# Optimization experiments

Measured on AMD Instinct MI355X. Metric: run time of the kernel, lower is better.

## Reference

```python
import jax, jax.numpy as jnp
import numpy as np

N_OCTAVES = 32
N_SAMPLES = 32768
SAMPLERATE = 22050
MIN_HZ = 20
MAX_HZ = 3000
BASE_RESONANCE = 0.01


def setup_inputs() -> dict:
    key = jax.random.key(0)
    k1, k2, k3 = jax.random.split(key, 3)
    B, E = 4, 16
    return {
        "f0": jax.random.uniform(k1, (B, E, 1), dtype=jnp.float32),
        "decay_coefficients": jax.random.normal(k2, (B, E, 1), dtype=jnp.float32),
        "freq_spacing": jax.random.uniform(k3, (B, E, 1), dtype=jnp.float32),
    }


def reference(f0, decay_coefficients, freq_spacing):
    B, E, _ = f0.shape
    min_freq = MIN_HZ / (SAMPLERATE // 2)
    max_freq = MAX_HZ / (SAMPLERATE // 2)
    freq_range = max_freq - min_freq

    f0 = jnp.abs(f0)  # (B, E, 1)

    # exponential_decay: note the forward applies sigmoid BEFORE calling
    # exponential_decay, which applies sigmoid again -> double sigmoid.
    dv = jax.nn.sigmoid(jax.nn.sigmoid(decay_coefficients))  # (B, E, 1)
    resonance_factor = (1.0 - BASE_RESONANCE) * 0.99
    d = BASE_RESONANCE + dv * resonance_factor  # (B, E, 1)
    log_d = jnp.broadcast_to(jnp.log(d + 1e-12), (B, E, N_OCTAVES))
    # interpolate(size=n_frames) with in==out size is the identity, so skip it.
    exp_decays = jnp.exp(jnp.cumsum(log_d, axis=-1))  # (B, E, O)

    f0 = (min_freq + f0 * freq_range) * np.pi  # (B, E, 1)
    factors = jnp.cumsum(jnp.broadcast_to(freq_spacing, (B, E, N_OCTAVES)), axis=-1)
    f0s = f0 * factors  # (B, E, O)
    f0s = f0s * (f0s < 1).astype(f0s.dtype)  # mask partials above Nyquist

    # cumsum of a constant per-sample frequency == freq * (sample_index + 1)
    t = jnp.arange(1, N_SAMPLES + 1, dtype=f0s.dtype)  # (S,)
    phase = f0s[..., None] * t  # (B, E, O, S)
    osc = jnp.sin(phase) * exp_decays[..., None]  # (B, E, O, S)

    osc = jnp.sum(osc, axis=2)  # (B, E, S)
    mx = jnp.max(jnp.abs(osc), axis=-1, keepdims=True)
    return osc / (mx + 1e-8)
```

## Files before the change

kernel.cpp:

```cpp
#include <hip/hip_runtime.h>
#include <math.h>

#define N_OCT  32
#define N_SMP  32768
#define N_PAIR 64
#define BPP    32

__global__ __launch_bounds__(256) void f0res_osc(
    const float* __restrict__ f0_in,
    const float* __restrict__ dec_in,
    const float* __restrict__ fs_in,
    float* __restrict__ out,
    float* __restrict__ bmax)
{
    __shared__ __align__(16) float sw[N_OCT];
    __shared__ __align__(16) float sa[N_OCT];
    __shared__ int s_ng;

    const int pair = blockIdx.x >> 5;
    const int blk  = blockIdx.x & (BPP - 1);
    const int tid  = threadIdx.x;

    if (tid < N_OCT) {
        const float minf   = (float)(20.0 / 11025.0);
        const float frange = (float)(3000.0 / 11025.0 - 20.0 / 11025.0);
        const float pif    = 3.14159265358979323846f;
        const float INV2PI = 0.15915494309189535f;

        float f0 = fabsf(f0_in[pair]);
        float fs = fs_in[pair];
        float x  = dec_in[pair];

        float s1 = 1.0f / (1.0f + expf(-x));
        float s2 = 1.0f / (1.0f + expf(-s1));
        float d  = 0.01f + s2 * (float)(0.99 * 0.99);
        float ld = logf(d + 1e-12f);
        float f0p = (minf + f0 * frange) * pif;

        float fac = 0.0f, acl = 0.0f, myfac = 0.0f, myacl = 0.0f;
#pragma unroll
        for (int o = 0; o < N_OCT; ++o) {
            fac += fs;
            acl += ld;
            if (o == tid) { myfac = fac; myacl = acl; }
        }
        float f0s = f0p * myfac;
        const bool act = (f0s < 1.0f);
        sw[tid] = act ? f0s * INV2PI : 0.0f;
        sa[tid] = expf(myacl);

        unsigned long long bal = __ballot(act);
        if (tid == 0) s_ng = (__popcll(bal) + 3) >> 2;
    }
    __syncthreads();

    const int ng = s_ng;

    const int   s0 = (blk << 10) + tid;
    const float t0 = (float)(s0 + 1);
    const float t1 = (float)(s0 + 257);
    const float t2 = (float)(s0 + 513);
    const float t3 = (float)(s0 + 769);

    float acc0 = 0.0f, acc1 = 0.0f, acc2 = 0.0f, acc3 = 0.0f;

    const float4* w4 = (const float4*)sw;
    const float4* a4 = (const float4*)sa;
    for (int i = 0; i < ng; ++i) {
        const float4 wv = w4[i];
        const float4 av = a4[i];
        const float wr[4] = { wv.x, wv.y, wv.z, wv.w };
        const float ar[4] = { av.x, av.y, av.z, av.w };
#pragma unroll
        for (int j = 0; j < 4; ++j) {
            const float w = wr[j], a = ar[j];
            acc0 = fmaf(a, __builtin_amdgcn_sinf(__builtin_amdgcn_fractf(w * t0)), acc0);
            acc1 = fmaf(a, __builtin_amdgcn_sinf(__builtin_amdgcn_fractf(w * t1)), acc1);
            acc2 = fmaf(a, __builtin_amdgcn_sinf(__builtin_amdgcn_fractf(w * t2)), acc2);
            acc3 = fmaf(a, __builtin_amdgcn_sinf(__builtin_amdgcn_fractf(w * t3)), acc3);
        }
    }

    float* op = out + pair * N_SMP + s0;
    op[0]   = acc0;
    op[256] = acc1;
    op[512] = acc2;
    op[768] = acc3;

    float av_ = fmaxf(fmaxf(fabsf(acc0), fabsf(acc1)),
                      fmaxf(fabsf(acc2), fabsf(acc3)));
#pragma unroll
    for (int m = 32; m >= 1; m >>= 1)
        av_ = fmaxf(av_, __shfl_xor(av_, m, 64));
    __shared__ float wm[4];
    if ((tid & 63) == 0) wm[tid >> 6] = av_;
    __syncthreads();
    if (tid == 0)
        bmax[pair * BPP + blk] = fmaxf(fmaxf(wm[0], wm[1]), fmaxf(wm[2], wm[3]));
}

__global__ __launch_bounds__(256) void f0res_norm(
    float* __restrict__ out, const float* __restrict__ bmax)
{
    const int pair = blockIdx.x >> 5;
    const int tid  = threadIdx.x;

    float v = (tid < BPP) ? bmax[pair * BPP + tid] : 0.0f;
#pragma unroll
    for (int m = 16; m >= 1; m >>= 1)
        v = fmaxf(v, __shfl_xor(v, m, 64));
    __shared__ float smx;
    if (tid == 0) smx = v;
    __syncthreads();
    const float inv = 1.0f / (smx + 1e-8f);

    const int idx = ((blockIdx.x & 31) << 8) + tid;
    float4* o4 = (float4*)(out + pair * N_SMP);
    float4 val = o4[idx];
    val.x *= inv; val.y *= inv; val.z *= inv; val.w *= inv;
    o4[idx] = val;
}

extern "C" void kernel_launch(void* const* d_in, const int* in_sizes, int n_in,
                              void* d_out, int out_size, void* d_ws, size_t ws_size,
                              hipStream_t stream) {
    const float* f0  = (const float*)d_in[0];
    const float* dec = (const float*)d_in[1];
    const float* fs  = (const float*)d_in[2];
    float* out = (float*)d_out;

    float* bmax = (float*)d_ws;

    f0res_osc <<<N_PAIR * BPP, 256, 0, stream>>>(f0, dec, fs, out, bmax);
    f0res_norm<<<N_PAIR * 32,  256, 0, stream>>>(out, bmax);
}
```

Before: 69.66 us.

## Fuse oscillator and normalization into one cooperative kernel with grid sync

Merges the oscillator synthesis and normalization kernels into a single cooperative launch. Each block now computes 8 samples per thread and keeps them in registers. After a grid-wide sync it reads the per-pair maxima and writes the normalized output directly. This removes the second kernel launch and a full global read-modify-write of the output. In exchange it adds grid-sync overhead, requires all 1024 blocks to be co-resident, and halves the block count per pair.

```diff
diff --git a/kernel.cpp b/kernel.cpp
--- a/kernel.cpp
+++ b/kernel.cpp
@@ -1,12 +1,14 @@
 #include <hip/hip_runtime.h>
+#include <hip/hip_cooperative_groups.h>
 #include <math.h>
 
 #define N_OCT  32
 #define N_SMP  32768
 #define N_PAIR 64
-#define BPP    32
+#define BPP    16
+#define NBLK   (N_PAIR * BPP)
 
-__global__ __launch_bounds__(256) void f0res_osc(
+__global__ __launch_bounds__(256, 4) void f0res_fused(
     const float* __restrict__ f0_in,
     const float* __restrict__ dec_in,
     const float* __restrict__ fs_in,
@@ -16,8 +18,9 @@
     __shared__ __align__(16) float sw[N_OCT];
     __shared__ __align__(16) float sa[N_OCT];
     __shared__ int s_ng;
+    __shared__ float wm[4];
 
-    const int pair = blockIdx.x >> 5;
+    const int pair = blockIdx.x >> 4;
     const int blk  = blockIdx.x & (BPP - 1);
     const int tid  = threadIdx.x;
 
@@ -56,13 +59,13 @@
 
     const int ng = s_ng;
 
-    const int   s0 = (blk << 10) + tid;
-    const float t0 = (float)(s0 + 1);
-    const float t1 = (float)(s0 + 257);
-    const float t2 = (float)(s0 + 513);
-    const float t3 = (float)(s0 + 769);
-
-    float acc0 = 0.0f, acc1 = 0.0f, acc2 = 0.0f, acc3 = 0.0f;
+    const int s0 = (blk << 11) + tid;
+    float t[8], acc[8];
+#pragma unroll
+    for (int k = 0; k < 8; ++k) {
+        t[k]   = (float)(s0 + 1 + (k << 8));
+        acc[k] = 0.0f;
+    }
 
     const float4* w4 = (const float4*)sw;
     const float4* a4 = (const float4*)sa;
@@ -74,51 +77,39 @@
 #pragma unroll
         for (int j = 0; j < 4; ++j) {
             const float w = wr[j], a = ar[j];
-            acc0 = fmaf(a, __builtin_amdgcn_sinf(__builtin_amdgcn_fractf(w * t0)), acc0);
-            acc1 = fmaf(a, __builtin_amdgcn_sinf(__builtin_amdgcn_fractf(w * t1)), acc1);
-            acc2 = fmaf(a, __builtin_amdgcn_sinf(__builtin_amdgcn_fractf(w * t2)), acc2);
-            acc3 = fmaf(a, __builtin_amdgcn_sinf(__builtin_amdgcn_fractf(w * t3)), acc3);
+#pragma unroll
+            for (int k = 0; k < 8; ++k)
+                acc[k] = fmaf(a, __builtin_amdgcn_sinf(
+                                     __builtin_amdgcn_fractf(w * t[k])), acc[k]);
         }
     }
 
-    float* op = out + pair * N_SMP + s0;
-    op[0]   = acc0;
-    op[256] = acc1;
-    op[512] = acc2;
-    op[768] = acc3;
-
-    float av_ = fmaxf(fmaxf(fabsf(acc0), fabsf(acc1)),
-                      fmaxf(fabsf(acc2), fabsf(acc3)));
+    float av_ = 0.0f;
+#pragma unroll
+    for (int k = 0; k < 8; ++k) av_ = fmaxf(av_, fabsf(acc[k]));
 #pragma unroll
     for (int m = 32; m >= 1; m >>= 1)
         av_ = fmaxf(av_, __shfl_xor(av_, m, 64));
-    __shared__ float wm[4];
     if ((tid & 63) == 0) wm[tid >> 6] = av_;
     __syncthreads();
-    if (tid == 0)
-        bmax[pair * BPP + blk] = fmaxf(fmaxf(wm[0], wm[1]), fmaxf(wm[2], wm[3]));
-}
+    if (tid == 0) {
+        bmax[(pair << 4) + blk] =
+            fmaxf(fmaxf(wm[0], wm[1]), fmaxf(wm[2], wm[3]));
+        __threadfence();
+    }
 
-__global__ __launch_bounds__(256) void f0res_norm(
-    float* __restrict__ out, const float* __restrict__ bmax)
-{
-    const int pair = blockIdx.x >> 5;
-    const int tid  = threadIdx.x;
+    cooperative_groups::this_grid().sync();
 
-    float v = (tid < BPP) ? bmax[pair * BPP + tid] : 0.0f;
+    float v = bmax[(pair << 4) + (tid & 15)];
 #pragma unroll
-    for (int m = 16; m >= 1; m >>= 1)
+    for (int m = 8; m >= 1; m >>= 1)
         v = fmaxf(v, __shfl_xor(v, m, 64));
-    __shared__ float smx;
-    if (tid == 0) smx = v;
-    __syncthreads();
-    const float inv = 1.0f / (smx + 1e-8f);
+    const float inv = 1.0f / (v + 1e-8f);
 
-    const int idx = ((blockIdx.x & 31) << 8) + tid;
-    float4* o4 = (float4*)(out + pair * N_SMP);
-    float4 val = o4[idx];
-    val.x *= inv; val.y *= inv; val.z *= inv; val.w *= inv;
-    o4[idx] = val;
+    float* op = out + pair * N_SMP + s0;
+#pragma unroll
+    for (int k = 0; k < 8; ++k)
+        op[k << 8] = acc[k] * inv;
 }
 
 extern "C" void kernel_launch(void* const* d_in, const int* in_sizes, int n_in,
@@ -127,10 +118,11 @@
     const float* f0  = (const float*)d_in[0];
     const float* dec = (const float*)d_in[1];
     const float* fs  = (const float*)d_in[2];
-    float* out = (float*)d_out;
-
+    float* out  = (float*)d_out;
     float* bmax = (float*)d_ws;
 
-    f0res_osc <<<N_PAIR * BPP, 256, 0, stream>>>(f0, dec, fs, out, bmax);
-    f0res_norm<<<N_PAIR * 32,  256, 0, stream>>>(out, bmax);
+    void* args[] = { (void*)&f0, (void*)&dec, (void*)&fs,
+                     (void*)&out, (void*)&bmax };
+    hipLaunchCooperativeKernel((void*)f0res_fused,
+                               dim3(NBLK), dim3(256), args, 0, stream);
 }
```

New measurement: 145.3 us. 2.09x slower.

## Fuse normalization into oscillator kernel via last-block atomic counter

Applied to the files above, without the earlier changes.

Drops the separate normalization kernel launch. Each block publishes its block max and increments a per-pair atomic counter, and the last block to finish for a pair reduces the maxima and rescales the whole 32K-sample row. The counter is reset by subtracting 32, and a probe value read from the workspace serves as the baseline. The aim is to remove launch overhead and the global barrier between kernels. In exchange, the rescale of each row is serialized onto a single block, and correctness depends on the workspace counter state and memory ordering.

```diff
diff --git a/kernel.cpp b/kernel.cpp
--- a/kernel.cpp
+++ b/kernel.cpp
@@ -11,15 +11,25 @@
     const float* __restrict__ dec_in,
     const float* __restrict__ fs_in,
     float* __restrict__ out,
-    float* __restrict__ bmax)
+    unsigned int* __restrict__ ws)
 {
     __shared__ __align__(16) float sw[N_OCT];
     __shared__ __align__(16) float sa[N_OCT];
     __shared__ int s_ng;
+    __shared__ unsigned int s_P;
+    __shared__ float wm[4];
+    __shared__ int s_last;
+    __shared__ float s_inv;
 
     const int pair = blockIdx.x >> 5;
     const int blk  = blockIdx.x & (BPP - 1);
     const int tid  = threadIdx.x;
+
+    unsigned int* cnt   = ws;
+    float*        bmax  = (float*)(ws + 256);
+    const unsigned int* probe = ws + (1u << 18);
+
+    if (tid == 0) s_P = probe[0];
 
     if (tid < N_OCT) {
         const float minf   = (float)(20.0 / 11025.0);
@@ -82,43 +92,60 @@
     }
 
     float* op = out + pair * N_SMP + s0;
-    op[0]   = acc0;
-    op[256] = acc1;
-    op[512] = acc2;
-    op[768] = acc3;
+    __hip_atomic_store(op + 0,   acc0, __ATOMIC_RELAXED, __HIP_MEMORY_SCOPE_AGENT);
+    __hip_atomic_store(op + 256, acc1, __ATOMIC_RELAXED, __HIP_MEMORY_SCOPE_AGENT);
+    __hip_atomic_store(op + 512, acc2, __ATOMIC_RELAXED, __HIP_MEMORY_SCOPE_AGENT);
+    __hip_atomic_store(op + 768, acc3, __ATOMIC_RELAXED, __HIP_MEMORY_SCOPE_AGENT);
 
     float av_ = fmaxf(fmaxf(fabsf(acc0), fabsf(acc1)),
                       fmaxf(fabsf(acc2), fabsf(acc3)));
 #pragma unroll
     for (int m = 32; m >= 1; m >>= 1)
         av_ = fmaxf(av_, __shfl_xor(av_, m, 64));
-    __shared__ float wm[4];
     if ((tid & 63) == 0) wm[tid >> 6] = av_;
+
+    asm volatile("s_waitcnt vmcnt(0)" ::: "memory");
     __syncthreads();
-    if (tid == 0)
-        bmax[pair * BPP + blk] = fmaxf(fmaxf(wm[0], wm[1]), fmaxf(wm[2], wm[3]));
-}
 
-__global__ __launch_bounds__(256) void f0res_norm(
-    float* __restrict__ out, const float* __restrict__ bmax)
-{
-    const int pair = blockIdx.x >> 5;
-    const int tid  = threadIdx.x;
+    if (tid == 0) {
+        float bm = fmaxf(fmaxf(wm[0], wm[1]), fmaxf(wm[2], wm[3]));
+        __hip_atomic_store(&bmax[(pair << 5) + blk], bm,
+                           __ATOMIC_RELAXED, __HIP_MEMORY_SCOPE_AGENT);
+        asm volatile("s_waitcnt vmcnt(0)" ::: "memory");
+        unsigned int old = atomicAdd(&cnt[pair], 1u);
+        s_last = (old == s_P + 31u);
+    }
+    __syncthreads();
 
-    float v = (tid < BPP) ? bmax[pair * BPP + tid] : 0.0f;
+    if (!s_last) return;
+
+    asm volatile("" ::: "memory");
+
+    if (tid < 64) {
+        float v = (tid < 32) ? bmax[(pair << 5) + tid] : 0.0f;
 #pragma unroll
-    for (int m = 16; m >= 1; m >>= 1)
-        v = fmaxf(v, __shfl_xor(v, m, 64));
-    __shared__ float smx;
-    if (tid == 0) smx = v;
+        for (int m = 16; m >= 1; m >>= 1)
+            v = fmaxf(v, __shfl_xor(v, m, 64));
+        if (tid == 0) s_inv = 1.0f / (v + 1e-8f);
+    }
     __syncthreads();
-    const float inv = 1.0f / (smx + 1e-8f);
+    const float inv = s_inv;
 
-    const int idx = ((blockIdx.x & 31) << 8) + tid;
     float4* o4 = (float4*)(out + pair * N_SMP);
-    float4 val = o4[idx];
-    val.x *= inv; val.y *= inv; val.z *= inv; val.w *= inv;
-    o4[idx] = val;
+#pragma unroll
+    for (int g = 0; g < 4; ++g) {
+        float4 v[8];
+#pragma unroll
+        for (int j = 0; j < 8; ++j)
+            v[j] = o4[tid + (((g << 3) + j) << 8)];
+#pragma unroll
+        for (int j = 0; j < 8; ++j) {
+            v[j].x *= inv; v[j].y *= inv; v[j].z *= inv; v[j].w *= inv;
+            o4[tid + (((g << 3) + j) << 8)] = v[j];
+        }
+    }
+
+    if (tid == 0) atomicAdd(&cnt[pair], (unsigned int)-32);
 }
 
 extern "C" void kernel_launch(void* const* d_in, const int* in_sizes, int n_in,
@@ -128,9 +155,7 @@
     const float* dec = (const float*)d_in[1];
     const float* fs  = (const float*)d_in[2];
     float* out = (float*)d_out;
+    unsigned int* ws = (unsigned int*)d_ws;
 
-    float* bmax = (float*)d_ws;
-
-    f0res_osc <<<N_PAIR * BPP, 256, 0, stream>>>(f0, dec, fs, out, bmax);
-    f0res_norm<<<N_PAIR * 32,  256, 0, stream>>>(out, bmax);
+    f0res_osc<<<N_PAIR * BPP, 256, 0, stream>>>(f0, dec, fs, out, ws);
 }
```

Result: slower. 95.16 us (+36.6%).
